# Optimization experiments

Measured on AMD Instinct MI355X. Metric: run time of the kernel, lower is better.

## Reference

```python
import jax, jax.numpy as jnp
import numpy as np

N_NODES = 100000


def _gcn_norm(edge_index, num_nodes):
    # add self loops
    src, dst = edge_index[0], edge_index[1]
    loop = jnp.arange(num_nodes, dtype=src.dtype)
    row = jnp.concatenate([src, loop])  # [E+N]
    col = jnp.concatenate([dst, loop])
    ew = jnp.ones(row.shape[0], dtype=jnp.float32)
    deg = jax.ops.segment_sum(ew, col, num_segments=num_nodes)  # [N]
    dinv = jnp.where(deg > 0, jax.lax.rsqrt(deg), 0.0)
    norm = dinv[row] * ew * dinv[col]  # [E+N]
    return row, col, norm


def setup_inputs() -> dict:
    key = jax.random.key(0)
    k1, k2, k3 = jax.random.split(key, 3)
    x = jax.random.normal(k1, (N_NODES, 64), dtype=jnp.float32)
    edge_index = jax.random.randint(k2, (2, 1280000), 0, N_NODES, dtype=jnp.int64)
    W = jax.random.normal(k3, (40, 64), dtype=jnp.float32) * (1.0 / np.sqrt(64))
    b = jnp.zeros((40,), dtype=jnp.float32)
    return {"x": x, "edge_index": edge_index, "W": W, "b": b}


def reference(x, edge_index, W, b):
    K = 3
    row, col, norm = _gcn_norm(edge_index, N_NODES)
    h = x
    for _ in range(K):
        # gather from source nodes, scale by symmetric norm, scatter-add to dst
        msg = norm[:, None] * h[row]  # [E+N, F]
        h = jax.ops.segment_sum(msg, col, num_segments=N_NODES)
    logits = h @ W.T + b  # [N, C]
    return jax.nn.log_softmax(logits, axis=1)
```

## Files before the change

### kernel.cpp

```cpp
#include <hip/hip_runtime.h>

#define F_IN 64
#define F_OUT 40
#define F4 10
#define USTRIDE 20

#define SCAN_BLK 256
#define SCAN_ELEMS 4
#define SCAN_TILE (SCAN_BLK * SCAN_ELEMS)

#define PART_BLK 256
#define PART_EPB 16
#define PART_TILE (PART_BLK * PART_EPB)
#define BSHIFT 8
#define BCAP 4096
#define MAXB 400

__device__ inline unsigned pk2(float x, float y) {
    unsigned a = __float_as_uint(x); a = (a + 0x7FFFu + ((a >> 16) & 1u)) >> 16;
    unsigned b = __float_as_uint(y); b = (b + 0x7FFFu + ((b >> 16) & 1u)) >> 16;
    return a | (b << 16);
}
__device__ inline void up4(uint2 u, float& a, float& b, float& c, float& d) {
    a = __uint_as_float(u.x << 16); b = __uint_as_float(u.x & 0xFFFF0000u);
    c = __uint_as_float(u.y << 16); d = __uint_as_float(u.y & 0xFFFF0000u);
}

__global__ __launch_bounds__(PART_BLK) void partition_kernel(const int* __restrict__ src,
                                                             const int* __restrict__ dst,
                                                             int* __restrict__ bfill,
                                                             unsigned* __restrict__ staging,
                                                             int E, int nbk) {
    __shared__ int hist[MAXB];
    __shared__ int base[MAXB];
    int tid = threadIdx.x;
    for (int b = tid; b < nbk; b += PART_BLK) hist[b] = 0;
    __syncthreads();

    int rank[PART_EPB];
    int bk[PART_EPB];
    unsigned rec[PART_EPB];
    int eb = blockIdx.x * PART_TILE + tid;
#pragma unroll
    for (int k = 0; k < PART_EPB; ++k) {
        int e = eb + k * PART_BLK;
        if (e < E) {
            int r = src[e];
            int c = dst[e];
            int b = c >> BSHIFT;
            bk[k] = b;
            rec[k] = (unsigned)r | ((unsigned)(c & 255) << 17);
            rank[k] = atomicAdd(&hist[b], 1);
        } else {
            bk[k] = -1;
        }
    }
    __syncthreads();
    for (int b = tid; b < nbk; b += PART_BLK) {
        int h = hist[b];
        base[b] = h ? atomicAdd(&bfill[b], h) : 0;
    }
    __syncthreads();
#pragma unroll
    for (int k = 0; k < PART_EPB; ++k) {
        if (bk[k] >= 0) staging[base[bk[k]] + rank[k]] = rec[k];
    }
}

__global__ __launch_bounds__(256) void bucket_deg_kernel(const unsigned* __restrict__ staging,
                                                         const int* __restrict__ bfill,
                                                         int* __restrict__ deg, int n) {
    int b = blockIdx.x;
    __shared__ int h[256];
    int tid = threadIdx.x;
    h[tid] = 0;
    __syncthreads();
    int cnt = bfill[b] - b * BCAP;
    const unsigned* rec = staging + (size_t)b * BCAP;
    for (int i = tid; i < cnt; i += 256) {
        atomicAdd(&h[rec[i] >> 17], 1);
    }
    __syncthreads();
    int node = (b << BSHIFT) | tid;
    if (node < n) deg[node] = h[tid];
}

__global__ void dinv_kernel(const int* __restrict__ deg, float* __restrict__ dinv,
                            float* __restrict__ dinv2, int n) {
    int i = blockIdx.x * blockDim.x + threadIdx.x;
    if (i >= n) return;
    float r = rsqrtf((float)deg[i] + 1.0f);
    dinv[i] = r;
    dinv2[i] = r * r;
}

__global__ __launch_bounds__(SCAN_BLK) void scan_a_kernel(const int* __restrict__ deg,
                                                          int* __restrict__ bsum, int n) {
    __shared__ int s[SCAN_BLK];
    int tid = threadIdx.x;
    int base = blockIdx.x * SCAN_TILE + tid * SCAN_ELEMS;
    int local = 0;
#pragma unroll
    for (int k = 0; k < SCAN_ELEMS; ++k) {
        int i = base + k;
        if (i < n) local += deg[i];
    }
    s[tid] = local;
    __syncthreads();
    for (int off = SCAN_BLK / 2; off > 0; off >>= 1) {
        if (tid < off) s[tid] += s[tid + off];
        __syncthreads();
    }
    if (tid == 0) bsum[blockIdx.x] = s[0];
}

__global__ __launch_bounds__(256) void scan_b_kernel(int* __restrict__ bsum,
                                                     int* __restrict__ total_out, int nb) {
    __shared__ int s[256];
    int tid = threadIdx.x;
    int v = (tid < nb) ? bsum[tid] : 0;
    s[tid] = v;
    __syncthreads();
    for (int off = 1; off < 256; off <<= 1) {
        int t = (tid >= off) ? s[tid - off] : 0;
        __syncthreads();
        s[tid] += t;
        __syncthreads();
    }
    if (tid < nb) bsum[tid] = s[tid] - v;
    if (tid == 255) *total_out = s[255];
}

__global__ __launch_bounds__(SCAN_BLK) void scan_c_kernel(const int* __restrict__ deg,
                                                          const int* __restrict__ boff,
                                                          int* __restrict__ rowptr, int n) {
    __shared__ int s[SCAN_BLK];
    int tid = threadIdx.x;
    int base = blockIdx.x * SCAN_TILE + tid * SCAN_ELEMS;
    int vals[SCAN_ELEMS];
    int local = 0;
#pragma unroll
    for (int k = 0; k < SCAN_ELEMS; ++k) {
        int i = base + k;
        vals[k] = (i < n) ? deg[i] : 0;
        local += vals[k];
    }
    s[tid] = local;
    __syncthreads();
    for (int off = 1; off < SCAN_BLK; off <<= 1) {
        int t = (tid >= off) ? s[tid - off] : 0;
        __syncthreads();
        s[tid] += t;
        __syncthreads();
    }
    int prefix = boff[blockIdx.x] + s[tid] - local;
#pragma unroll
    for (int k = 0; k < SCAN_ELEMS; ++k) {
        int i = base + k;
        if (i < n) {
            rowptr[i] = prefix;
            prefix += vals[k];
        }
    }
}

__global__ __launch_bounds__(256) void bucket_scatter_kernel(const unsigned* __restrict__ staging,
                                                             const int* __restrict__ bfill,
                                                             const int* __restrict__ rowptr,
                                                             int* __restrict__ srcs, int n) {
    int b = blockIdx.x;
    __shared__ int cur[256];
    int tid = threadIdx.x;
    int node = (b << BSHIFT) | tid;
    cur[tid] = (node < n) ? rowptr[node] : 0;
    __syncthreads();
    int cnt = bfill[b] - b * BCAP;
    const unsigned* rec = staging + (size_t)b * BCAP;
    for (int i = tid; i < cnt; i += 256) {
        unsigned r = rec[i];
        int pos = atomicAdd(&cur[r >> 17], 1);
        srcs[pos] = (int)(r & 0x1FFFFu);
    }
}

__global__ __launch_bounds__(256) void proj_kernel(const float* __restrict__ x,
                                                   const float* __restrict__ W,
                                                   const float* __restrict__ dinv,
                                                   unsigned* __restrict__ u, int n) {
    __shared__ float Ws[F_OUT * F_IN];
    for (int i = threadIdx.x; i < F_OUT * F_IN; i += blockDim.x) Ws[i] = W[i];
    __syncthreads();

    int node = blockIdx.x * blockDim.x + threadIdx.x;
    if (node >= n) return;

    const float4* xp  = (const float4*)(x + (size_t)node * F_IN);
    const float4* Ws4 = (const float4*)Ws;

    float acc[F_OUT];
#pragma unroll
    for (int c = 0; c < F_OUT; ++c) acc[c] = 0.0f;
#pragma unroll
    for (int f4 = 0; f4 < F_IN / 4; ++f4) {
        float4 xv = xp[f4];
#pragma unroll
        for (int c = 0; c < F_OUT; ++c) {
            float4 w = Ws4[c * (F_IN / 4) + f4];
            acc[c] += xv.x * w.x + xv.y * w.y + xv.z * w.z + xv.w * w.w;
        }
    }
    float dv = dinv[node];
    uint4* up = (uint4*)(u + (size_t)node * USTRIDE);
#pragma unroll
    for (int g = 0; g < 5; ++g) {
        uint4 o;
        o.x = pk2(dv * acc[8 * g + 0], dv * acc[8 * g + 1]);
        o.y = pk2(dv * acc[8 * g + 2], dv * acc[8 * g + 3]);
        o.z = pk2(dv * acc[8 * g + 4], dv * acc[8 * g + 5]);
        o.w = pk2(dv * acc[8 * g + 6], dv * acc[8 * g + 7]);
        up[g] = o;
    }
}

__global__ __launch_bounds__(256) void propagate_kernel(const int* __restrict__ rowptr,
                                                        const int* __restrict__ srcs,
                                                        const float* __restrict__ dinv2,
                                                        const unsigned* __restrict__ ucur,
                                                        unsigned* __restrict__ unew, int n) {
    int t = blockIdx.x * blockDim.x + threadIdx.x;
    int node = t / F4;
    int q = t - node * F4;
    if (node >= n) return;

    int beg = rowptr[node];
    int end = rowptr[node + 1];

    const uint2* U = (const uint2*)ucur;
    float ax, ay, az, aw;
    up4(U[(size_t)node * F4 + q], ax, ay, az, aw);

    int i = beg;
    for (; i + 3 < end; i += 4) {
        int s0 = srcs[i], s1 = srcs[i + 1], s2 = srcs[i + 2], s3 = srcs[i + 3];
        uint2 v0 = U[(size_t)s0 * F4 + q];
        uint2 v1 = U[(size_t)s1 * F4 + q];
        uint2 v2 = U[(size_t)s2 * F4 + q];
        uint2 v3 = U[(size_t)s3 * F4 + q];
        float b0, b1, b2, b3;
        up4(v0, b0, b1, b2, b3); ax += b0; ay += b1; az += b2; aw += b3;
        up4(v1, b0, b1, b2, b3); ax += b0; ay += b1; az += b2; aw += b3;
        up4(v2, b0, b1, b2, b3); ax += b0; ay += b1; az += b2; aw += b3;
        up4(v3, b0, b1, b2, b3); ax += b0; ay += b1; az += b2; aw += b3;
    }
    for (; i < end; ++i) {
        float b0, b1, b2, b3;
        up4(U[(size_t)srcs[i] * F4 + q], b0, b1, b2, b3);
        ax += b0; ay += b1; az += b2; aw += b3;
    }

    float ds = dinv2[node];
    uint2 o;
    o.x = pk2(ds * ax, ds * ay);
    o.y = pk2(ds * az, ds * aw);
    ((uint2*)unew)[(size_t)node * F4 + q] = o;
}

__global__ void logsoftmax_kernel(const unsigned* __restrict__ u, float* __restrict__ out,
                                  const float* __restrict__ bias,
                                  const int* __restrict__ deg, int n) {
    int node = blockIdx.x * blockDim.x + threadIdx.x;
    if (node >= n) return;
    float sq = sqrtf((float)deg[node] + 1.0f);
    const uint4* up = (const uint4*)(u + (size_t)node * USTRIDE);
    float v[F_OUT];
#pragma unroll
    for (int g = 0; g < 5; ++g) {
        uint4 t = up[g];
        float a, b, c, d;
        up4(make_uint2(t.x, t.y), a, b, c, d);
        v[8 * g + 0] = sq * a + bias[8 * g + 0];
        v[8 * g + 1] = sq * b + bias[8 * g + 1];
        v[8 * g + 2] = sq * c + bias[8 * g + 2];
        v[8 * g + 3] = sq * d + bias[8 * g + 3];
        up4(make_uint2(t.z, t.w), a, b, c, d);
        v[8 * g + 4] = sq * a + bias[8 * g + 4];
        v[8 * g + 5] = sq * b + bias[8 * g + 5];
        v[8 * g + 6] = sq * c + bias[8 * g + 6];
        v[8 * g + 7] = sq * d + bias[8 * g + 7];
    }
    float mx = -1e30f;
#pragma unroll
    for (int c = 0; c < F_OUT; ++c) mx = fmaxf(mx, v[c]);
    float se = 0.0f;
#pragma unroll
    for (int c = 0; c < F_OUT; ++c) se += __expf(v[c] - mx);
    float lse = mx + __logf(se);
    float4* p = (float4*)(out + (size_t)node * F_OUT);
#pragma unroll
    for (int c4 = 0; c4 < F4; ++c4) {
        float4 t;
        t.x = v[4 * c4 + 0] - lse; t.y = v[4 * c4 + 1] - lse;
        t.z = v[4 * c4 + 2] - lse; t.w = v[4 * c4 + 3] - lse;
        p[c4] = t;
    }
}

__global__ void bucket_init_kernel(int* __restrict__ bfill, int nbk) {
    int b = blockIdx.x * blockDim.x + threadIdx.x;
    if (b < nbk) bfill[b] = b * BCAP;
}

extern "C" void kernel_launch(void* const* d_in, const int* in_sizes, int n_in,
                              void* d_out, int out_size, void* d_ws, size_t ws_size,
                              hipStream_t stream) {
    const float* x  = (const float*)d_in[0];
    const int*   ei = (const int*)d_in[1];
    const float* W  = (const float*)d_in[2];
    const float* b  = (const float*)d_in[3];

    const int N = in_sizes[0] / F_IN;
    const int E = in_sizes[1] / 2;
    const int* src = ei;
    const int* dst = ei + E;
    const int nbk = (N + (1 << BSHIFT) - 1) >> BSHIFT;

    char* base = (char*)d_ws;
    size_t off = 0;
    auto alloc = [&](size_t bytes) {
        char* p = base + off;
        off = (off + bytes + 255) & ~(size_t)255;
        return p;
    };
    int*      deg_i   = (int*)     alloc((size_t)N * 4);
    float*    dinv    = (float*)   alloc((size_t)N * 4);
    float*    dinv2   = (float*)   alloc((size_t)N * 4);
    int*      rowptr  = (int*)     alloc((size_t)(N + 1) * 4);
    int*      bsum    = (int*)     alloc(256 * 4);
    int*      bfill   = (int*)     alloc((size_t)MAXB * 4);
    unsigned* staging = (unsigned*)alloc((size_t)nbk * BCAP * 4);
    int*      srcs_s  = (int*)     alloc((size_t)E * 4);
    unsigned* uA      = (unsigned*)alloc((size_t)N * USTRIDE * 4);
    unsigned* uB      = (unsigned*)alloc((size_t)N * USTRIDE * 4);
    float*    outp    = (float*)d_out;

    const int nb = (N + SCAN_TILE - 1) / SCAN_TILE;

    bucket_init_kernel<<<(nbk + 255) / 256, 256, 0, stream>>>(bfill, nbk);
    partition_kernel<<<(E + PART_TILE - 1) / PART_TILE, PART_BLK, 0, stream>>>(
        src, dst, bfill, staging, E, nbk);

    bucket_deg_kernel<<<nbk, 256, 0, stream>>>(staging, bfill, deg_i, N);
    dinv_kernel<<<(N + 255) / 256, 256, 0, stream>>>(deg_i, dinv, dinv2, N);

    scan_a_kernel<<<nb, SCAN_BLK, 0, stream>>>(deg_i, bsum, N);
    scan_b_kernel<<<1, 256, 0, stream>>>(bsum, rowptr + N, nb);
    scan_c_kernel<<<nb, SCAN_BLK, 0, stream>>>(deg_i, bsum, rowptr, N);

    bucket_scatter_kernel<<<nbk, 256, 0, stream>>>(staging, bfill, rowptr, srcs_s, N);

    proj_kernel<<<(N + 255) / 256, 256, 0, stream>>>(x, W, dinv, uA, N);

    const int pt = N * F4;
    const int pg = (pt + 255) / 256;
    propagate_kernel<<<pg, 256, 0, stream>>>(rowptr, srcs_s, dinv2, uA, uB, N);
    propagate_kernel<<<pg, 256, 0, stream>>>(rowptr, srcs_s, dinv2, uB, uA, N);
    propagate_kernel<<<pg, 256, 0, stream>>>(rowptr, srcs_s, dinv2, uA, uB, N);

    logsoftmax_kernel<<<(N + 255) / 256, 256, 0, stream>>>(uB, outp, b, deg_i, N);
}
```

Measured before the change: 247.4 us.

## Fuse CSR build into per-bucket finalize kernel and widen propagate gathers to 16 bytes

```diff
diff --git a/kernel.cpp b/kernel.cpp
--- a/kernel.cpp
+++ b/kernel.cpp
@@ -2,28 +2,28 @@
 
 #define F_IN 64
 #define F_OUT 40
-#define F4 10
 #define USTRIDE 20
-
-#define SCAN_BLK 256
-#define SCAN_ELEMS 4
-#define SCAN_TILE (SCAN_BLK * SCAN_ELEMS)
+#define QPN 5
 
 #define PART_BLK 256
 #define PART_EPB 16
 #define PART_TILE (PART_BLK * PART_EPB)
 #define BSHIFT 8
 #define BCAP 4096
-#define MAXB 400
+#define MAXB 512
 
 __device__ inline unsigned pk2(float x, float y) {
     unsigned a = __float_as_uint(x); a = (a + 0x7FFFu + ((a >> 16) & 1u)) >> 16;
     unsigned b = __float_as_uint(y); b = (b + 0x7FFFu + ((b >> 16) & 1u)) >> 16;
     return a | (b << 16);
 }
-__device__ inline void up4(uint2 u, float& a, float& b, float& c, float& d) {
-    a = __uint_as_float(u.x << 16); b = __uint_as_float(u.x & 0xFFFF0000u);
-    c = __uint_as_float(u.y << 16); d = __uint_as_float(u.y & 0xFFFF0000u);
+__device__ inline void up2(unsigned u, float& a, float& b) {
+    a = __uint_as_float(u << 16); b = __uint_as_float(u & 0xFFFF0000u);
+}
+
+__global__ void bucket_init_kernel(int* __restrict__ bfill, int nbk) {
+    int b = blockIdx.x * blockDim.x + threadIdx.x;
+    if (b < nbk) bfill[b] = b * BCAP;
 }
 
 __global__ __launch_bounds__(PART_BLK) void partition_kernel(const int* __restrict__ src,
@@ -67,119 +67,71 @@
     }
 }
 
-__global__ __launch_bounds__(256) void bucket_deg_kernel(const unsigned* __restrict__ staging,
-                                                         const int* __restrict__ bfill,
-                                                         int* __restrict__ deg, int n) {
+__global__ __launch_bounds__(512) void btotal_scan_kernel(const int* __restrict__ bfill,
+                                                          int* __restrict__ ebase,
+                                                          int* __restrict__ rowptr_end,
+                                                          int nbk, int E) {
+    __shared__ int s[512];
+    int tid = threadIdx.x;
+    int v = (tid < nbk) ? (bfill[tid] - tid * BCAP) : 0;
+    s[tid] = v;
+    __syncthreads();
+    for (int off = 1; off < 512; off <<= 1) {
+        int t = (tid >= off) ? s[tid - off] : 0;
+        __syncthreads();
+        s[tid] += t;
+        __syncthreads();
+    }
+    if (tid < nbk) ebase[tid] = s[tid] - v;
+    if (tid == 0) *rowptr_end = E;
+}
+
+__global__ __launch_bounds__(256) void bucket_finalize_kernel(const unsigned* __restrict__ staging,
+                                                              const int* __restrict__ bfill,
+                                                              const int* __restrict__ ebase,
+                                                              int* __restrict__ rowptr,
+                                                              int* __restrict__ deg,
+                                                              float* __restrict__ dinv,
+                                                              float* __restrict__ dinv2,
+                                                              int* __restrict__ srcs, int n) {
     int b = blockIdx.x;
     __shared__ int h[256];
+    __shared__ int cur[256];
     int tid = threadIdx.x;
     h[tid] = 0;
     __syncthreads();
+
     int cnt = bfill[b] - b * BCAP;
     const unsigned* rec = staging + (size_t)b * BCAP;
     for (int i = tid; i < cnt; i += 256) {
         atomicAdd(&h[rec[i] >> 17], 1);
     }
     __syncthreads();
+
+    int v = h[tid];
+    for (int off = 1; off < 256; off <<= 1) {
+        int t = (tid >= off) ? h[tid - off] : 0;
+        __syncthreads();
+        h[tid] += t;
+        __syncthreads();
+    }
+    int excl = h[tid] - v;
+    int base = ebase[b];
     int node = (b << BSHIFT) | tid;
-    if (node < n) deg[node] = h[tid];
-}
-
-__global__ void dinv_kernel(const int* __restrict__ deg, float* __restrict__ dinv,
-                            float* __restrict__ dinv2, int n) {
-    int i = blockIdx.x * blockDim.x + threadIdx.x;
-    if (i >= n) return;
-    float r = rsqrtf((float)deg[i] + 1.0f);
-    dinv[i] = r;
-    dinv2[i] = r * r;
-}
-
-__global__ __launch_bounds__(SCAN_BLK) void scan_a_kernel(const int* __restrict__ deg,
-                                                          int* __restrict__ bsum, int n) {
-    __shared__ int s[SCAN_BLK];
-    int tid = threadIdx.x;
-    int base = blockIdx.x * SCAN_TILE + tid * SCAN_ELEMS;
-    int local = 0;
-#pragma unroll
-    for (int k = 0; k < SCAN_ELEMS; ++k) {
-        int i = base + k;
-        if (i < n) local += deg[i];
-    }
-    s[tid] = local;
-    __syncthreads();
-    for (int off = SCAN_BLK / 2; off > 0; off >>= 1) {
-        if (tid < off) s[tid] += s[tid + off];
-        __syncthreads();
-    }
-    if (tid == 0) bsum[blockIdx.x] = s[0];
-}
-
-__global__ __launch_bounds__(256) void scan_b_kernel(int* __restrict__ bsum,
-                                                     int* __restrict__ total_out, int nb) {
-    __shared__ int s[256];
-    int tid = threadIdx.x;
-    int v = (tid < nb) ? bsum[tid] : 0;
-    s[tid] = v;
-    __syncthreads();
-    for (int off = 1; off < 256; off <<= 1) {
-        int t = (tid >= off) ? s[tid - off] : 0;
-        __syncthreads();
-        s[tid] += t;
-        __syncthreads();
-    }
-    if (tid < nb) bsum[tid] = s[tid] - v;
-    if (tid == 255) *total_out = s[255];
-}
-
-__global__ __launch_bounds__(SCAN_BLK) void scan_c_kernel(const int* __restrict__ deg,
-                                                          const int* __restrict__ boff,
-                                                          int* __restrict__ rowptr, int n) {
-    __shared__ int s[SCAN_BLK];
-    int tid = threadIdx.x;
-    int base = blockIdx.x * SCAN_TILE + tid * SCAN_ELEMS;
-    int vals[SCAN_ELEMS];
-    int local = 0;
-#pragma unroll
-    for (int k = 0; k < SCAN_ELEMS; ++k) {
-        int i = base + k;
-        vals[k] = (i < n) ? deg[i] : 0;
-        local += vals[k];
-    }
-    s[tid] = local;
-    __syncthreads();
-    for (int off = 1; off < SCAN_BLK; off <<= 1) {
-        int t = (tid >= off) ? s[tid - off] : 0;
-        __syncthreads();
-        s[tid] += t;
-        __syncthreads();
-    }
-    int prefix = boff[blockIdx.x] + s[tid] - local;
-#pragma unroll
-    for (int k = 0; k < SCAN_ELEMS; ++k) {
-        int i = base + k;
-        if (i < n) {
-            rowptr[i] = prefix;
-            prefix += vals[k];
-        }
-    }
-}
-
-__global__ __launch_bounds__(256) void bucket_scatter_kernel(const unsigned* __restrict__ staging,
-                                                             const int* __restrict__ bfill,
-                                                             const int* __restrict__ rowptr,
-                                                             int* __restrict__ srcs, int n) {
-    int b = blockIdx.x;
-    __shared__ int cur[256];
-    int tid = threadIdx.x;
-    int node = (b << BSHIFT) | tid;
-    cur[tid] = (node < n) ? rowptr[node] : 0;
-    __syncthreads();
-    int cnt = bfill[b] - b * BCAP;
-    const unsigned* rec = staging + (size_t)b * BCAP;
+    if (node < n) {
+        rowptr[node] = base + excl;
+        deg[node] = v;
+        float r = rsqrtf((float)v + 1.0f);
+        dinv[node] = r;
+        dinv2[node] = r * r;
+    }
+    cur[tid] = base + excl;
+    __syncthreads();
+
     for (int i = tid; i < cnt; i += 256) {
-        unsigned r = rec[i];
-        int pos = atomicAdd(&cur[r >> 17], 1);
-        srcs[pos] = (int)(r & 0x1FFFFu);
+        unsigned rv = rec[i];
+        int pos = atomicAdd(&cur[rv >> 17], 1);
+        srcs[pos] = (int)(rv & 0x1FFFFu);
     }
 }
 
@@ -228,41 +180,59 @@
                                                         const unsigned* __restrict__ ucur,
                                                         unsigned* __restrict__ unew, int n) {
     int t = blockIdx.x * blockDim.x + threadIdx.x;
-    int node = t / F4;
-    int q = t - node * F4;
+    int node = t / QPN;
+    int q = t - node * QPN;
     if (node >= n) return;
 
     int beg = rowptr[node];
     int end = rowptr[node + 1];
 
-    const uint2* U = (const uint2*)ucur;
-    float ax, ay, az, aw;
-    up4(U[(size_t)node * F4 + q], ax, ay, az, aw);
+    const uint4* U = (const uint4*)ucur;
+    uint4 sv = U[(size_t)node * QPN + q];
+    float a0, a1, a2, a3, a4, a5, a6, a7;
+    up2(sv.x, a0, a1); up2(sv.y, a2, a3); up2(sv.z, a4, a5); up2(sv.w, a6, a7);
 
     int i = beg;
     for (; i + 3 < end; i += 4) {
         int s0 = srcs[i], s1 = srcs[i + 1], s2 = srcs[i + 2], s3 = srcs[i + 3];
-        uint2 v0 = U[(size_t)s0 * F4 + q];
-        uint2 v1 = U[(size_t)s1 * F4 + q];
-        uint2 v2 = U[(size_t)s2 * F4 + q];
-        uint2 v3 = U[(size_t)s3 * F4 + q];
-        float b0, b1, b2, b3;
-        up4(v0, b0, b1, b2, b3); ax += b0; ay += b1; az += b2; aw += b3;
-        up4(v1, b0, b1, b2, b3); ax += b0; ay += b1; az += b2; aw += b3;
-        up4(v2, b0, b1, b2, b3); ax += b0; ay += b1; az += b2; aw += b3;
-        up4(v3, b0, b1, b2, b3); ax += b0; ay += b1; az += b2; aw += b3;
+        uint4 v0 = U[(size_t)s0 * QPN + q];
+        uint4 v1 = U[(size_t)s1 * QPN + q];
+        uint4 v2 = U[(size_t)s2 * QPN + q];
+        uint4 v3 = U[(size_t)s3 * QPN + q];
+        float b0, b1;
+        up2(v0.x, b0, b1); a0 += b0; a1 += b1;
+        up2(v0.y, b0, b1); a2 += b0; a3 += b1;
+        up2(v0.z, b0, b1); a4 += b0; a5 += b1;
+        up2(v0.w, b0, b1); a6 += b0; a7 += b1;
+        up2(v1.x, b0, b1); a0 += b0; a1 += b1;
+        up2(v1.y, b0, b1); a2 += b0; a3 += b1;
+        up2(v1.z, b0, b1); a4 += b0; a5 += b1;
+        up2(v1.w, b0, b1); a6 += b0; a7 += b1;
+        up2(v2.x, b0, b1); a0 += b0; a1 += b1;
+        up2(v2.y, b0, b1); a2 += b0; a3 += b1;
+        up2(v2.z, b0, b1); a4 += b0; a5 += b1;
+        up2(v2.w, b0, b1); a6 += b0; a7 += b1;
+        up2(v3.x, b0, b1); a0 += b0; a1 += b1;
+        up2(v3.y, b0, b1); a2 += b0; a3 += b1;
+        up2(v3.z, b0, b1); a4 += b0; a5 += b1;
+        up2(v3.w, b0, b1); a6 += b0; a7 += b1;
     }
     for (; i < end; ++i) {
-        float b0, b1, b2, b3;
-        up4(U[(size_t)srcs[i] * F4 + q], b0, b1, b2, b3);
-        ax += b0; ay += b1; az += b2; aw += b3;
+        uint4 v = U[(size_t)srcs[i] * QPN + q];
+        float b0, b1;
+        up2(v.x, b0, b1); a0 += b0; a1 += b1;
+        up2(v.y, b0, b1); a2 += b0; a3 += b1;
+        up2(v.z, b0, b1); a4 += b0; a5 += b1;
+        up2(v.w, b0, b1); a6 += b0; a7 += b1;
     }
 
     float ds = dinv2[node];
-    uint2 o;
-    o.x = pk2(ds * ax, ds * ay);
-    o.y = pk2(ds * az, ds * aw);
-    ((uint2*)unew)[(size_t)node * F4 + q] = o;
+    uint4 o;
+    o.x = pk2(ds * a0, ds * a1);
+    o.y = pk2(ds * a2, ds * a3);
+    o.z = pk2(ds * a4, ds * a5);
+    o.w = pk2(ds * a6, ds * a7);
+    ((uint4*)unew)[(size_t)node * QPN + q] = o;
 }
 
 __global__ void logsoftmax_kernel(const unsigned* __restrict__ u, float* __restrict__ out,
@@ -276,17 +246,15 @@
 #pragma unroll
     for (int g = 0; g < 5; ++g) {
         uint4 t = up[g];
-        float a, b, c, d;
-        up4(make_uint2(t.x, t.y), a, b, c, d);
-        v[8 * g + 0] = sq * a + bias[8 * g + 0];
-        v[8 * g + 1] = sq * b + bias[8 * g + 1];
-        v[8 * g + 2] = sq * c + bias[8 * g + 2];
-        v[8 * g + 3] = sq * d + bias[8 * g + 3];
-        up4(make_uint2(t.z, t.w), a, b, c, d);
-        v[8 * g + 4] = sq * a + bias[8 * g + 4];
-        v[8 * g + 5] = sq * b + bias[8 * g + 5];
-        v[8 * g + 6] = sq * c + bias[8 * g + 6];
-        v[8 * g + 7] = sq * d + bias[8 * g + 7];
+        float a, b2;
+        up2(t.x, a, b2); v[8 * g + 0] = sq * a + bias[8 * g + 0];
+                         v[8 * g + 1] = sq * b2 + bias[8 * g + 1];
+        up2(t.y, a, b2); v[8 * g + 2] = sq * a + bias[8 * g + 2];
+                         v[8 * g + 3] = sq * b2 + bias[8 * g + 3];
+        up2(t.z, a, b2); v[8 * g + 4] = sq * a + bias[8 * g + 4];
+                         v[8 * g + 5] = sq * b2 + bias[8 * g + 5];
+        up2(t.w, a, b2); v[8 * g + 6] = sq * a + bias[8 * g + 6];
+                         v[8 * g + 7] = sq * b2 + bias[8 * g + 7];
     }
     float mx = -1e30f;
 #pragma unroll
@@ -297,17 +265,12 @@
     float lse = mx + __logf(se);
     float4* p = (float4*)(out + (size_t)node * F_OUT);
 #pragma unroll
-    for (int c4 = 0; c4 < F4; ++c4) {
+    for (int c4 = 0; c4 < F_OUT / 4; ++c4) {
         float4 t;
         t.x = v[4 * c4 + 0] - lse; t.y = v[4 * c4 + 1] - lse;
         t.z = v[4 * c4 + 2] - lse; t.w = v[4 * c4 + 3] - lse;
         p[c4] = t;
     }
-}
-
-__global__ void bucket_init_kernel(int* __restrict__ bfill, int nbk) {
-    int b = blockIdx.x * blockDim.x + threadIdx.x;
-    if (b < nbk) bfill[b] = b * BCAP;
 }
 
 extern "C" void kernel_launch(void* const* d_in, const int* in_sizes, int n_in,
@@ -335,32 +298,25 @@
     float*    dinv    = (float*)   alloc((size_t)N * 4);
     float*    dinv2   = (float*)   alloc((size_t)N * 4);
     int*      rowptr  = (int*)     alloc((size_t)(N + 1) * 4);
-    int*      bsum    = (int*)     alloc(256 * 4);
     int*      bfill   = (int*)     alloc((size_t)MAXB * 4);
+    int*      ebase   = (int*)     alloc((size_t)MAXB * 4);
     unsigned* staging = (unsigned*)alloc((size_t)nbk * BCAP * 4);
     int*      srcs_s  = (int*)     alloc((size_t)E * 4);
     unsigned* uA      = (unsigned*)alloc((size_t)N * USTRIDE * 4);
     unsigned* uB      = (unsigned*)alloc((size_t)N * USTRIDE * 4);
     float*    outp    = (float*)d_out;
 
-    const int nb = (N + SCAN_TILE - 1) / SCAN_TILE;
-
     bucket_init_kernel<<<(nbk + 255) / 256, 256, 0, stream>>>(bfill, nbk);
     partition_kernel<<<(E + PART_TILE - 1) / PART_TILE, PART_BLK, 0, stream>>>(
         src, dst, bfill, staging, E, nbk);
 
-    bucket_deg_kernel<<<nbk, 256, 0, stream>>>(staging, bfill, deg_i, N);
-    dinv_kernel<<<(N + 255) / 256, 256, 0, stream>>>(deg_i, dinv, dinv2, N);
-
-    scan_a_kernel<<<nb, SCAN_BLK, 0, stream>>>(deg_i, bsum, N);
-    scan_b_kernel<<<1, 256, 0, stream>>>(bsum, rowptr + N, nb);
-    scan_c_kernel<<<nb, SCAN_BLK, 0, stream>>>(deg_i, bsum, rowptr, N);
-
-    bucket_scatter_kernel<<<nbk, 256, 0, stream>>>(staging, bfill, rowptr, srcs_s, N);
+    btotal_scan_kernel<<<1, 512, 0, stream>>>(bfill, ebase, rowptr + N, nbk, E);
+    bucket_finalize_kernel<<<nbk, 256, 0, stream>>>(staging, bfill, ebase, rowptr,
+                                                    deg_i, dinv, dinv2, srcs_s, N);
 
     proj_kernel<<<(N + 255) / 256, 256, 0, stream>>>(x, W, dinv, uA, N);
 
-    const int pt = N * F4;
+    const int pt = N * QPN;
     const int pg = (pt + 255) / 256;
     propagate_kernel<<<pg, 256, 0, stream>>>(rowptr, srcs_s, dinv2, uA, uB, N);
     propagate_kernel<<<pg, 256, 0, stream>>>(rowptr, srcs_s, dinv2, uB, uA, N);
```

New measurement: 237.7 us. 3.9% less time.
